# Performance work log

Measured on AMD Instinct MI355X. Metric: run time of the kernel, lower is better.

Reference implementation:

```python
import jax, jax.numpy as jnp
import numpy as np

B, N, QD = 1, 4096, 1024
H, DH = 16, 64  # heads, dim_head; inner_dim = H*DH = 1024
SCALE = DH ** -0.5


def setup_inputs() -> dict:
    key = jax.random.key(0)
    ks = jax.random.split(key, 6)
    inner = H * DH
    return {
        "x": jax.random.normal(ks[0], (B, N, QD), dtype=jnp.float32),
        "Wq": jax.random.normal(ks[1], (QD, inner), dtype=jnp.float32) * (QD ** -0.5),
        "Wk": jax.random.normal(ks[2], (QD, inner), dtype=jnp.float32) * (QD ** -0.5),
        "Wv": jax.random.normal(ks[3], (QD, inner), dtype=jnp.float32) * (QD ** -0.5),
        "Wo": jax.random.normal(ks[4], (inner, QD), dtype=jnp.float32) * (inner ** -0.5),
        "bo": jnp.zeros((QD,), dtype=jnp.float32),
    }


def reference(x, Wq, Wk, Wv, Wo, bo):
    b, n, _ = x.shape
    # projections, split heads: b n (h d) -> b h n d
    q = (x @ Wq).reshape(b, n, H, DH).transpose(0, 2, 1, 3)
    k = (x @ Wk).reshape(b, n, H, DH).transpose(0, 2, 1, 3)
    v = (x @ Wv).reshape(b, n, H, DH).transpose(0, 2, 1, 3)
    # fp32-forced QK^T (ATTN_PRECISION='fp32' path), then scale
    sim = jnp.einsum("bhid,bhjd->bhij", q.astype(jnp.float32), k.astype(jnp.float32)) * SCALE
    attn = jax.nn.softmax(sim, axis=-1)
    out = jnp.einsum("bhij,bhjd->bhid", attn, v)  # b h n d
    out = out.transpose(0, 2, 1, 3).reshape(b, n, H * DH)  # merge heads
    return out @ Wo + bo
```

## Files before the change

### kernel.cpp

```cpp
#include <hip/hip_runtime.h>
#include <stdint.h>

#define NH 16
#define NN 4096

typedef __attribute__((ext_vector_type(8))) short bf16x8;
typedef __attribute__((ext_vector_type(4))) short bf16x4;
typedef __attribute__((ext_vector_type(4))) float f32x4;
typedef __attribute__((ext_vector_type(16))) float f32x16;
typedef unsigned short u16;
typedef unsigned int u32;
typedef __attribute__((ext_vector_type(4))) u32 u32x4;

__device__ __forceinline__ u16 f2bf(float f) {
  u32 u = __float_as_uint(f);
  return (u16)((u + 0x7FFFu + ((u >> 16) & 1u)) >> 16);
}

#define GLD16(gp, lp)                                              \
  __builtin_amdgcn_global_load_lds(                                \
      (__attribute__((address_space(1))) void*)(gp),               \
      (__attribute__((address_space(3))) void*)(lp), 16, 0, 0)

__global__ __launch_bounds__(256) void prep(const float* __restrict__ x,
                                            const float* __restrict__ Wq,
                                            const float* __restrict__ Wk,
                                            const float* __restrict__ Wv,
                                            const float* __restrict__ Wo,
                                            u16* __restrict__ xb,
                                            u16* __restrict__ Wqt, u16* __restrict__ Wkt,
                                            u16* __restrict__ Wvt, u16* __restrict__ Wot) {
  __shared__ float tile[64][65];
  int z = blockIdx.z;
  int tid = threadIdx.x;
  if (z >= 4) {
    int bi = (z - 4) * 256 + blockIdx.y * 16 + blockIdx.x;
    size_t base = (size_t)bi * 8192;
#pragma unroll
    for (int k = 0; k < 4; ++k) {
      size_t i = base + (size_t)k * 2048 + tid * 8;
      float4 a = *(const float4*)(x + i);
      float4 b = *(const float4*)(x + i + 4);
      uint4 o;
      o.x = (u32)f2bf(a.x) | ((u32)f2bf(a.y) << 16);
      o.y = (u32)f2bf(a.z) | ((u32)f2bf(a.w) << 16);
      o.z = (u32)f2bf(b.x) | ((u32)f2bf(b.y) << 16);
      o.w = (u32)f2bf(b.z) | ((u32)f2bf(b.w) << 16);
      *(uint4*)(xb + i) = o;
    }
    return;
  }
  const float* src;
  u16* dst;
  float scale = 1.0f;
  if (z == 0) { src = Wq; dst = Wqt; scale = 0.125f * 1.4426950408889634f; }
  else if (z == 1) { src = Wk; dst = Wkt; }
  else if (z == 2) { src = Wv; dst = Wvt; }
  else { src = Wo; dst = Wot; }
  int tx = tid & 63, ty = tid >> 6;
  int c0 = blockIdx.x * 64, r0 = blockIdx.y * 64;
#pragma unroll
  for (int i = ty; i < 64; i += 4)
    tile[i][tx] = src[(size_t)(r0 + i) * 1024 + c0 + tx];
  __syncthreads();
#pragma unroll
  for (int i = ty; i < 64; i += 4)
    dst[(size_t)(c0 + i) * 1024 + r0 + tx] = f2bf(tile[tx][i] * scale);
}

__global__ __launch_bounds__(256) void gemm_qkv(const u16* __restrict__ A,
                                                const u16* __restrict__ Bt,
                                                u16* __restrict__ Qb, u16* __restrict__ Kb,
                                                u16* __restrict__ Vth) {
  __shared__ __align__(16) u16 SH[16384];
  u16* A_lds = SH;
  u16* B_lds = SH + 8192;
  const int tid = threadIdx.x;
  const int l = tid & 63, w = tid >> 6;
  const int g = l >> 4, c = l & 15;
  const int wr = w >> 1, wc = w & 1;
  const int m0 = blockIdx.y * 128, n0 = blockIdx.x * 128;

  const int srow = tid >> 2;
  const u32 sswz = (u32)(((tid & 3) * 16) ^ ((srow & 3) << 4));
  const char* Ag = (const char*)A + (size_t)(m0 + srow) * 2048 + sswz;
  const char* Bg = (const char*)Bt + (size_t)(n0 + srow) * 2048 + sswz;
  const u32 ldsb = (u32)(w * 1024);

#define GSTAGE(buf, ks_)                                                          \
  do {                                                                            \
    u32 koff_ = (u32)(ks_) * 64;                                                  \
    _Pragma("unroll") for (int p_ = 0; p_ < 2; ++p_) {                            \
      GLD16(Ag + koff_ + (size_t)p_ * 64 * 2048,                                  \
            (char*)A_lds + (buf) * 8192 + p_ * 4096 + ldsb);                      \
      GLD16(Bg + koff_ + (size_t)p_ * 64 * 2048,                                  \
            (char*)B_lds + (buf) * 8192 + p_ * 4096 + ldsb);                      \
    }                                                                             \
  } while (0)

  f32x4 acc[4][4];
#pragma unroll
  for (int i = 0; i < 4; ++i)
#pragma unroll
    for (int j = 0; j < 4; ++j) acc[i][j] = (f32x4){0.f, 0.f, 0.f, 0.f};

  int cur = 0;
  GSTAGE(0, 0);
  for (int ks = 0; ks < 32; ++ks) {
    GSTAGE(cur ^ 1, (ks + 1) & 31);
    asm volatile("s_waitcnt vmcnt(4)" ::: "memory");
    __builtin_amdgcn_s_barrier();
    __builtin_amdgcn_sched_barrier(0);
    const char* Ac = (const char*)A_lds + cur * 8192;
    const char* Bc = (const char*)B_lds + cur * 8192;
    bf16x8 af[4], bfr[4];
#pragma unroll
    for (int i = 0; i < 4; ++i) {
      int row = wr * 64 + i * 16 + c;
      af[i] = *(const bf16x8*)(Ac + row * 64 + ((g * 16) ^ ((row & 3) << 4)));
    }
#pragma unroll
    for (int j = 0; j < 4; ++j) {
      int row = wc * 64 + j * 16 + c;
      bfr[j] = *(const bf16x8*)(Bc + row * 64 + ((g * 16) ^ ((row & 3) << 4)));
    }
    __builtin_amdgcn_s_setprio(1);
#pragma unroll
    for (int i = 0; i < 4; ++i)
#pragma unroll
      for (int j = 0; j < 4; ++j)
        acc[i][j] = __builtin_amdgcn_mfma_f32_16x16x32_bf16(af[i], bfr[j], acc[i][j], 0, 0, 0);
    __builtin_amdgcn_s_setprio(0);
    asm volatile("s_waitcnt lgkmcnt(0)" ::: "memory");
    __builtin_amdgcn_s_barrier();
    __builtin_amdgcn_sched_barrier(0);
    cur ^= 1;
  }
#undef GSTAGE

  const int sec = n0 >> 10;
  if (sec < 2) {
#pragma unroll
    for (int i = 0; i < 4; ++i)
#pragma unroll
      for (int j = 0; j < 4; ++j)
#pragma unroll
        for (int r = 0; r < 4; ++r) {
          int m = m0 + wr * 64 + i * 16 + g * 4 + r;
          int cc = (n0 + wc * 64 + j * 16 + c) & 1023;
          u16 v = f2bf(acc[i][j][r]);
          if (sec == 0) Qb[(size_t)m * 1024 + cc] = v;
          else Kb[(size_t)m * 1024 + cc] = v;
        }
  } else {
    const int gq = ((g & 1) << 1) | (g >> 1);
    const int cc0 = n0 & 1023;
#pragma unroll
    for (int i = 0; i < 4; ++i)
#pragma unroll
      for (int j = 0; j < 4; ++j)
#pragma unroll
        for (int r = 0; r < 4; ++r) {
          int cl = wc * 64 + j * 16 + c;
          int mql = wr * 64 + i * 16 + gq * 4 + r;
          SH[cl * 128 + (mql ^ ((cl & 15) << 3))] = f2bf(acc[i][j][r]);
        }
    __syncthreads();
#pragma unroll
    for (int p = 0; p < 4; ++p) {
      int row = p * 32 + (tid >> 3);
#pragma unroll
      for (int half = 0; half < 2; ++half) {
        int mq = (tid & 7) * 8 + half * 64;
        bf16x8 vv = *(const bf16x8*)&SH[row * 128 + (mq ^ ((row & 15) << 3))];
        *(bf16x8*)(Vth + (size_t)(cc0 + row) * 4096 + m0 + mq) = vv;
      }
    }
  }
}

__global__ __launch_bounds__(256) void gemm_out128(const u16* __restrict__ A,
                                                   const u16* __restrict__ Bt,
                                                   float* __restrict__ out,
                                                   const float* __restrict__ bias) {
  __shared__ __align__(16) u16 A_lds[2][128 * 32];
  __shared__ __align__(16) u16 B_lds[2][64 * 32];
  const int tid = threadIdx.x;
  const int l = tid & 63, w = tid >> 6;
  const int g = l >> 4, c = l & 15;
  const int m0 = blockIdx.y * 128, n0 = blockIdx.x * 64;

  const int srow = tid >> 2;
  const u32 sswz = (u32)(((tid & 3) * 16) ^ ((srow & 3) << 4));
  const char* Ag = (const char*)A + (size_t)(m0 + srow) * 2048 + sswz;
  const char* Bg = (const char*)Bt + (size_t)(n0 + srow) * 2048 + sswz;
  const u32 ldsb = (u32)(w * 1024);

#define GSTAGE3(buf, ks_)                                                         \
  do {                                                                            \
    u32 koff_ = (u32)(ks_) * 64;                                                  \
    GLD16(Ag + koff_, (char*)A_lds[buf] + ldsb);                                  \
    GLD16(Ag + koff_ + (size_t)64 * 2048, (char*)A_lds[buf] + 4096 + ldsb);       \
    GLD16(Bg + koff_, (char*)B_lds[buf] + ldsb);                                  \
  } while (0)

  f32x4 acc[2][4];
#pragma unroll
  for (int i = 0; i < 2; ++i)
#pragma unroll
    for (int j = 0; j < 4; ++j) acc[i][j] = (f32x4){0.f, 0.f, 0.f, 0.f};

  int cur = 0;
  GSTAGE3(0, 0);
  for (int ks = 0; ks < 32; ++ks) {
    GSTAGE3(cur ^ 1, (ks + 1) & 31);
    asm volatile("s_waitcnt vmcnt(3)" ::: "memory");
    __builtin_amdgcn_s_barrier();
    __builtin_amdgcn_sched_barrier(0);
    const char* Ac = (const char*)A_lds[cur];
    const char* Bc = (const char*)B_lds[cur];
    bf16x8 af[2], bfr[4];
#pragma unroll
    for (int i = 0; i < 2; ++i) {
      int row = w * 32 + i * 16 + c;
      af[i] = *(const bf16x8*)(Ac + row * 64 + ((g * 16) ^ ((row & 3) << 4)));
    }
#pragma unroll
    for (int j = 0; j < 4; ++j) {
      int row = j * 16 + c;
      bfr[j] = *(const bf16x8*)(Bc + row * 64 + ((g * 16) ^ ((row & 3) << 4)));
    }
    __builtin_amdgcn_s_setprio(1);
#pragma unroll
    for (int i = 0; i < 2; ++i)
#pragma unroll
      for (int j = 0; j < 4; ++j)
        acc[i][j] = __builtin_amdgcn_mfma_f32_16x16x32_bf16(af[i], bfr[j], acc[i][j], 0, 0, 0);
    __builtin_amdgcn_s_setprio(0);
    asm volatile("s_waitcnt lgkmcnt(0)" ::: "memory");
    __builtin_amdgcn_s_barrier();
    __builtin_amdgcn_sched_barrier(0);
    cur ^= 1;
  }
#undef GSTAGE3

#pragma unroll
  for (int i = 0; i < 2; ++i)
#pragma unroll
    for (int j = 0; j < 4; ++j)
#pragma unroll
      for (int r = 0; r < 4; ++r) {
        int m = m0 + w * 32 + i * 16 + g * 4 + r;
        int col = n0 + j * 16 + c;
        out[(size_t)m * 1024 + col] = acc[i][j][r] + bias[col];
      }
}

template <int SPLIT>
__global__ __launch_bounds__(256, 2) void flash_attn_t(const u16* __restrict__ Qb,
                                                       const u16* __restrict__ Kb,
                                                       const u16* __restrict__ Vt,
                                                       u16* __restrict__ Ob,
                                                       float* __restrict__ Op,
                                                       float* __restrict__ Lp) {
  constexpr int NT = SPLIT ? 32 : 64;
  __shared__ __align__(16) u16 K_lds[2][64 * 64];
  __shared__ __align__(16) u16 V_lds[2][64 * 64];
  const int tid = threadIdx.x;
  const int l = tid & 63, w = tid >> 6;
  const int lq = l & 31, hi = l >> 5;
  const int h = blockIdx.y;
  const int z = SPLIT ? blockIdx.z : 0;
  const int kb = z * 32;
  const int qb = blockIdx.x * 256 + w * 64;
  const int q0 = qb + lq, q1 = qb + 32 + lq;

  bf16x8 qf0[4], qf1[4];
  {
    const u16* qr0 = Qb + (size_t)q0 * 1024 + h * 64;
    const u16* qr1 = Qb + (size_t)q1 * 1024 + h * 64;
#pragma unroll
    for (int dm = 0; dm < 4; ++dm) {
      qf0[dm] = *(const bf16x8*)(qr0 + dm * 16 + hi * 8);
      qf1[dm] = *(const bf16x8*)(qr1 + dm * 16 + hi * 8);
    }
  }

  f32x16 ot0[2], ot1[2];
#pragma unroll
  for (int a = 0; a < 2; ++a)
#pragma unroll
    for (int r = 0; r < 16; ++r) { ot0[a][r] = 0.f; ot1[a][r] = 0.f; }
  float lrow0 = 0.f, lrow1 = 0.f;
  u32 pkA0[16], pkA1[16], pkB0[16], pkB1[16];

  const int srow = tid >> 3;
  const u32 sswz = (u32)(((tid & 7) * 16) ^ ((srow & 7) << 4));
  const char* Kg = (const char*)Kb + ((size_t)srow * 1024 + h * 64) * 2 + sswz;
  const char* Vg = (const char*)Vt + ((size_t)(h * 64 + srow) * 4096) * 2 + sswz;
  const u32 ldsb = (u32)(w * 1024);

#define PVONLY(P0, P1, VSLOT)                                                     \
  {                                                                               \
    const char* Vp_ = (const char*)(VSLOT);                                       \
    __builtin_amdgcn_s_setprio(1);                                                \
    _Pragma("unroll") for (int sti_ = 0; sti_ < 4; ++sti_) {                      \
      u32x4 pw0_ = {P0[sti_ * 4 + 0], P0[sti_ * 4 + 1], P0[sti_ * 4 + 2],         \
                    P0[sti_ * 4 + 3]};                                            \
      u32x4 pw1_ = {P1[sti_ * 4 + 0], P1[sti_ * 4 + 1], P1[sti_ * 4 + 2],         \
                    P1[sti_ * 4 + 3]};                                            \
      bf16x8 pf0_ = __builtin_bit_cast(bf16x8, pw0_);                             \
      bf16x8 pf1_ = __builtin_bit_cast(bf16x8, pw1_);                             \
      const u32 cb_ = (u32)(sti_ * 32 + hi * 16);                                 \
      _Pragma("unroll") for (int a_ = 0; a_ < 2; ++a_) {                          \
        const int rowd_ = a_ * 32 + lq;                                           \
        const u32 rs_ = (u32)(rowd_ * 128), rz_ = (u32)((rowd_ & 7) << 4);        \
        bf16x8 vf_ = *(const bf16x8*)(Vp_ + rs_ + (cb_ ^ rz_));                   \
        ot0[a_] = __builtin_amdgcn_mfma_f32_32x32x16_bf16(vf_, pf0_, ot0[a_], 0, 0, 0); \
        ot1[a_] = __builtin_amdgcn_mfma_f32_32x32x16_bf16(vf_, pf1_, ot1[a_], 0, 0, 0); \
      }                                                                           \
    }                                                                             \
    __builtin_amdgcn_s_setprio(0);                                                \
  }

#define BODY(TI, C0, C1, P0, P1, DOPREV)                                          \
  {                                                                               \
    const int ti_ = (TI);                                                         \
    const int nxt_ = (ti_ + 1) & (NT - 1);                                        \
    {                                                                             \
      const char* kg_ = Kg + (size_t)(kb + nxt_) * 64 * 2048;                     \
      char* kl_ = (char*)K_lds[nxt_ & 1] + ldsb;                                  \
      GLD16(kg_, kl_);                                                            \
      GLD16(kg_ + 32 * 2048, kl_ + 4096);                                         \
      const char* vg_ = Vg + (size_t)(kb + ti_) * 128;                            \
      char* vl_ = (char*)V_lds[ti_ & 1] + ldsb;                                   \
      GLD16(vg_, vl_);                                                            \
      GLD16(vg_ + (size_t)32 * 8192, vl_ + 4096);                                 \
    }                                                                             \
    asm volatile("s_waitcnt vmcnt(4)" ::: "memory");                              \
    __builtin_amdgcn_s_barrier();                                                 \
    __builtin_amdgcn_sched_barrier(0);                                            \
    const char* Kc_ = (const char*)K_lds[ti_ & 1];                                \
    f32x16 st0_[2], st1_[2];                                                      \
    _Pragma("unroll") for (int s_ = 0; s_ < 2; ++s_)                              \
    _Pragma("unroll") for (int r_ = 0; r_ < 16; ++r_) {                           \
      st0_[s_][r_] = 0.f;                                                         \
      st1_[s_][r_] = 0.f;                                                         \
    }                                                                             \
    __builtin_amdgcn_s_setprio(1);                                                \
    _Pragma("unroll") for (int s_ = 0; s_ < 2; ++s_) {                            \
      const int row_ = s_ * 32 + lq;                                              \
      const u32 rs_ = (u32)(row_ * 128), rz_ = (u32)((row_ & 7) << 4);            \
      _Pragma("unroll") for (int dm_ = 0; dm_ < 4; ++dm_) {                       \
        bf16x8 kf_ = *(const bf16x8*)(Kc_ + rs_ + ((u32)(dm_ * 32 + hi * 16) ^ rz_)); \
        st0_[s_] = __builtin_amdgcn_mfma_f32_32x32x16_bf16(kf_, qf0[dm_], st0_[s_], 0, 0, 0); \
        st1_[s_] = __builtin_amdgcn_mfma_f32_32x32x16_bf16(kf_, qf1[dm_], st1_[s_], 0, 0, 0); \
      }                                                                           \
    }                                                                             \
    __builtin_amdgcn_s_setprio(0);                                                \
    if (DOPREV) PVONLY(P0, P1, V_lds[(ti_ - 1) & 1]);                             \
    float rs0_ = 0.f, rs1_ = 0.f;                                                 \
    _Pragma("unroll") for (int s_ = 0; s_ < 2; ++s_)                              \
    _Pragma("unroll") for (int j_ = 0; j_ < 8; ++j_) {                            \
      float a0_ = __builtin_amdgcn_exp2f(st0_[s_][2 * j_]);                       \
      float a1_ = __builtin_amdgcn_exp2f(st0_[s_][2 * j_ + 1]);                   \
      rs0_ += a0_ + a1_;                                                          \
      u32 wp0_;                                                                   \
      asm("v_cvt_pk_bf16_f32 %0, %1, %2" : "=v"(wp0_) : "v"(a0_), "v"(a1_));      \
      C0[s_ * 8 + j_] = wp0_;                                                     \
      float b0_ = __builtin_amdgcn_exp2f(st1_[s_][2 * j_]);                       \
      float b1_ = __builtin_amdgcn_exp2f(st1_[s_][2 * j_ + 1]);                   \
      rs1_ += b0_ + b1_;                                                          \
      u32 wp1_;                                                                   \
      asm("v_cvt_pk_bf16_f32 %0, %1, %2" : "=v"(wp1_) : "v"(b0_), "v"(b1_));      \
      C1[s_ * 8 + j_] = wp1_;                                                     \
    }                                                                             \
    lrow0 += rs0_;                                                                \
    lrow1 += rs1_;                                                                \
    asm volatile("s_waitcnt lgkmcnt(0)" ::: "memory");                            \
    __builtin_amdgcn_s_barrier();                                                 \
    __builtin_amdgcn_sched_barrier(0);                                            \
  }

  {
    const char* kg0 = Kg + (size_t)kb * 64 * 2048;
    char* kl = (char*)K_lds[0] + ldsb;
    GLD16(kg0, kl);
    GLD16(kg0 + 32 * 2048, kl + 4096);
  }

  BODY(0, pkA0, pkA1, pkA0, pkA1, 0);
  for (int i = 1; i < NT - 1; i += 2) {
    BODY(i, pkB0, pkB1, pkA0, pkA1, 1);
    BODY(i + 1, pkA0, pkA1, pkB0, pkB1, 1);
  }
  BODY(NT - 1, pkB0, pkB1, pkA0, pkA1, 1);
  asm volatile("s_waitcnt vmcnt(0)" ::: "memory");
  __builtin_amdgcn_s_barrier();
  __builtin_amdgcn_sched_barrier(0);
  PVONLY(pkB0, pkB1, V_lds[(NT - 1) & 1]);

#undef BODY
#undef PVONLY

  lrow0 += __shfl_xor(lrow0, 32, 64);
  lrow1 += __shfl_xor(lrow1, 32, 64);
  if constexpr (SPLIT) {
    float* or0 = Op + (size_t)z * (4096 * 1024) + (size_t)q0 * 1024 + h * 64 + hi * 4;
    float* or1 = Op + (size_t)z * (4096 * 1024) + (size_t)q1 * 1024 + h * 64 + hi * 4;
#pragma unroll
    for (int a = 0; a < 2; ++a)
#pragma unroll
      for (int rr = 0; rr < 4; ++rr) {
        float4 f0 = {ot0[a][rr * 4 + 0], ot0[a][rr * 4 + 1], ot0[a][rr * 4 + 2],
                     ot0[a][rr * 4 + 3]};
        *(float4*)(or0 + a * 32 + rr * 8) = f0;
        float4 f1 = {ot1[a][rr * 4 + 0], ot1[a][rr * 4 + 1], ot1[a][rr * 4 + 2],
                     ot1[a][rr * 4 + 3]};
        *(float4*)(or1 + a * 32 + rr * 8) = f1;
      }
    if (hi == 0) {
      Lp[z * 65536 + h * 4096 + q0] = lrow0;
      Lp[z * 65536 + h * 4096 + q1] = lrow1;
    }
  } else {
    float inv0 = 1.f / lrow0, inv1 = 1.f / lrow1;
    u16* or0 = Ob + (size_t)q0 * 1024 + h * 64 + hi * 4;
    u16* or1 = Ob + (size_t)q1 * 1024 + h * 64 + hi * 4;
#pragma unroll
    for (int a = 0; a < 2; ++a)
#pragma unroll
      for (int rr = 0; rr < 4; ++rr) {
        ushort4 o4;
        o4.x = f2bf(ot0[a][rr * 4 + 0] * inv0);
        o4.y = f2bf(ot0[a][rr * 4 + 1] * inv0);
        o4.z = f2bf(ot0[a][rr * 4 + 2] * inv0);
        o4.w = f2bf(ot0[a][rr * 4 + 3] * inv0);
        *(ushort4*)(or0 + a * 32 + rr * 8) = o4;
        o4.x = f2bf(ot1[a][rr * 4 + 0] * inv1);
        o4.y = f2bf(ot1[a][rr * 4 + 1] * inv1);
        o4.z = f2bf(ot1[a][rr * 4 + 2] * inv1);
        o4.w = f2bf(ot1[a][rr * 4 + 3] * inv1);
        *(ushort4*)(or1 + a * 32 + rr * 8) = o4;
      }
  }
}

__global__ __launch_bounds__(256) void merge_halves(const float* __restrict__ O0,
                                                    const float* __restrict__ O1,
                                                    const float* __restrict__ L0,
                                                    const float* __restrict__ L1,
                                                    u16* __restrict__ Ob) {
  int idx = blockIdx.x * 256 + threadIdx.x;
  int q = idx >> 7;
  int c0 = (idx & 127) * 8;
  int h = c0 >> 6;
  float inv = 1.f / (L0[h * 4096 + q] + L1[h * 4096 + q]);
  size_t off = (size_t)q * 1024 + c0;
  float4 a0 = *(const float4*)(O0 + off), a1 = *(const float4*)(O0 + off + 4);
  float4 b0 = *(const float4*)(O1 + off), b1 = *(const float4*)(O1 + off + 4);
  ushort4 o0, o1;
  o0.x = f2bf((a0.x + b0.x) * inv);
  o0.y = f2bf((a0.y + b0.y) * inv);
  o0.z = f2bf((a0.z + b0.z) * inv);
  o0.w = f2bf((a0.w + b0.w) * inv);
  o1.x = f2bf((a1.x + b1.x) * inv);
  o1.y = f2bf((a1.y + b1.y) * inv);
  o1.z = f2bf((a1.z + b1.z) * inv);
  o1.w = f2bf((a1.w + b1.w) * inv);
  *(ushort4*)(Ob + off) = o0;
  *(ushort4*)(Ob + off + 4) = o1;
}

extern "C" void kernel_launch(void* const* d_in, const int* in_sizes, int n_in,
                              void* d_out, int out_size, void* d_ws, size_t ws_size,
                              hipStream_t stream) {
  const float* x = (const float*)d_in[0];
  const float* Wq = (const float*)d_in[1];
  const float* Wk = (const float*)d_in[2];
  const float* Wv = (const float*)d_in[3];
  const float* Wo = (const float*)d_in[4];
  const float* bo = (const float*)d_in[5];
  float* out = (float*)d_out;

  char* ws = (char*)d_ws;
  u16* xb  = (u16*)(ws);
  u16* Wqt = (u16*)(ws + (8u << 20));
  u16* Wot = (u16*)(ws + (14u << 20));
  u16* Qb  = (u16*)(ws + (16u << 20));
  u16* Kbf = (u16*)(ws + (24u << 20));
  u16* Vth = (u16*)(ws + (32u << 20));
  u16* Ob  = (u16*)(ws + (40u << 20));
  float* Op = (float*)(ws + (40u << 20));
  float* Lp = (float*)(ws + (72u << 20));
  u16* Wkt = Wqt + (1u << 20);
  u16* Wvt = Wqt + (2u << 20);

  const bool split = ws_size >= ((73u << 20) + (1u << 19));

  prep<<<dim3(16, 16, 6), 256, 0, stream>>>(x, Wq, Wk, Wv, Wo, xb, Wqt, Wkt, Wvt, Wot);
  gemm_qkv<<<dim3(24, 32), 256, 0, stream>>>(xb, Wqt, Qb, Kbf, Vth);

  if (split) {
    flash_attn_t<1><<<dim3(16, 16, 2), 256, 0, stream>>>(Qb, Kbf, Vth, nullptr, Op, Lp);
    u16* ObM = (u16*)ws;
    merge_halves<<<2048, 256, 0, stream>>>(Op, Op + (1u << 22), Lp, Lp + 65536, ObM);
    gemm_out128<<<dim3(16, 32), 256, 0, stream>>>(ObM, Wot, out, bo);
  } else {
    flash_attn_t<0><<<dim3(16, 16, 1), 256, 0, stream>>>(Qb, Kbf, Vth, Ob, nullptr, nullptr);
    gemm_out128<<<dim3(16, 32), 256, 0, stream>>>(Ob, Wot, out, bo);
  }
}
```

Measured before the change: 162.4 us.

## Fuse split-K attention merge into output GEMM and remap attention block order

Drops the separate merge_halves kernel. The output projection GEMM now reads the two fp32 partial attention outputs and their row sums directly, then combines, normalises and converts them to bf16 while staging its A tile into LDS. This saves one launch and the write and reread of the bf16 intermediate. The cost is that every N-tile block of the GEMM reloads the fp32 partials, which is 16x redundant global traffic, and does more ALU work inside the GEMM loop. Separately, the flash attention grid uses a new block-index swizzle that interleaves heads and splits across groups of 8, likely to spread K/V reuse across XCDs.

```diff
diff --git a/kernel.cpp b/kernel.cpp
--- a/kernel.cpp
+++ b/kernel.cpp
@@ -256,6 +256,135 @@
       }
 }
 
+__global__ __launch_bounds__(256) void gemm_out128f(const float* __restrict__ O0,
+                                                    const float* __restrict__ O1,
+                                                    const float* __restrict__ L0,
+                                                    const float* __restrict__ L1,
+                                                    const u16* __restrict__ Bt,
+                                                    float* __restrict__ out,
+                                                    const float* __restrict__ bias) {
+  __shared__ __align__(16) u16 A_lds[2][128 * 32];
+  __shared__ __align__(16) u16 B_lds[2][64 * 32];
+  const int tid = threadIdx.x;
+  const int l = tid & 63, w = tid >> 6;
+  const int g = l >> 4, c = l & 15;
+  const int m0 = blockIdx.y * 128, n0 = blockIdx.x * 64;
+
+  const int srow = tid >> 2;
+  const int chunk = tid & 3;
+  const int cidx = chunk ^ (srow & 3);
+  const u32 sswz = (u32)(((tid & 3) * 16) ^ ((srow & 3) << 4));
+  const char* Bg = (const char*)Bt + (size_t)(n0 + srow) * 2048 + sswz;
+  const u32 ldsb = (u32)(w * 1024);
+
+  float4 va0, va1, vb0, vb1, wa0, wa1, wb0, wb1;
+  float l0a, l1a, l0b, l1b;
+
+#define A_LOAD(KSN)                                                               \
+  {                                                                               \
+    int k0n_ = (KSN) * 32, hn_ = (KSN) >> 1;                                      \
+    const float* p0a_ = O0 + (size_t)(m0 + srow) * 1024 + k0n_ + cidx * 8;        \
+    const float* p0b_ = O0 + (size_t)(m0 + srow + 64) * 1024 + k0n_ + cidx * 8;   \
+    const float* p1a_ = O1 + (size_t)(m0 + srow) * 1024 + k0n_ + cidx * 8;        \
+    const float* p1b_ = O1 + (size_t)(m0 + srow + 64) * 1024 + k0n_ + cidx * 8;   \
+    va0 = *(const float4*)(p0a_);                                                 \
+    va1 = *(const float4*)(p0a_ + 4);                                             \
+    vb0 = *(const float4*)(p0b_);                                                 \
+    vb1 = *(const float4*)(p0b_ + 4);                                             \
+    wa0 = *(const float4*)(p1a_);                                                 \
+    wa1 = *(const float4*)(p1a_ + 4);                                             \
+    wb0 = *(const float4*)(p1b_);                                                 \
+    wb1 = *(const float4*)(p1b_ + 4);                                             \
+    l0a = L0[hn_ * 4096 + m0 + srow];                                             \
+    l1a = L1[hn_ * 4096 + m0 + srow];                                             \
+    l0b = L0[hn_ * 4096 + m0 + srow + 64];                                        \
+    l1b = L1[hn_ * 4096 + m0 + srow + 64];                                        \
+  }
+
+#define A_WRITE(BUF)                                                              \
+  {                                                                               \
+    float inva_ = 1.f / (l0a + l1a);                                              \
+    float invb_ = 1.f / (l0b + l1b);                                              \
+    uint4 pa_, pb_;                                                               \
+    pa_.x = (u32)f2bf((va0.x + wa0.x) * inva_) |                                  \
+            ((u32)f2bf((va0.y + wa0.y) * inva_) << 16);                           \
+    pa_.y = (u32)f2bf((va0.z + wa0.z) * inva_) |                                  \
+            ((u32)f2bf((va0.w + wa0.w) * inva_) << 16);                           \
+    pa_.z = (u32)f2bf((va1.x + wa1.x) * inva_) |                                  \
+            ((u32)f2bf((va1.y + wa1.y) * inva_) << 16);                           \
+    pa_.w = (u32)f2bf((va1.z + wa1.z) * inva_) |                                  \
+            ((u32)f2bf((va1.w + wa1.w) * inva_) << 16);                           \
+    pb_.x = (u32)f2bf((vb0.x + wb0.x) * invb_) |                                  \
+            ((u32)f2bf((vb0.y + wb0.y) * invb_) << 16);                           \
+    pb_.y = (u32)f2bf((vb0.z + wb0.z) * invb_) |                                  \
+            ((u32)f2bf((vb0.w + wb0.w) * invb_) << 16);                           \
+    pb_.z = (u32)f2bf((vb1.x + wb1.x) * invb_) |                                  \
+            ((u32)f2bf((vb1.y + wb1.y) * invb_) << 16);                           \
+    pb_.w = (u32)f2bf((vb1.z + wb1.z) * invb_) |                                  \
+            ((u32)f2bf((vb1.w + wb1.w) * invb_) << 16);                           \
+    *(uint4*)((char*)A_lds[BUF] + srow * 64 + chunk * 16) = pa_;                  \
+    *(uint4*)((char*)A_lds[BUF] + 4096 + srow * 64 + chunk * 16) = pb_;           \
+  }
+
+  f32x4 acc[2][4];
+#pragma unroll
+  for (int i = 0; i < 2; ++i)
+#pragma unroll
+    for (int j = 0; j < 4; ++j) acc[i][j] = (f32x4){0.f, 0.f, 0.f, 0.f};
+
+  GLD16(Bg, (char*)B_lds[0] + ldsb);
+  A_LOAD(0);
+  A_WRITE(0);
+
+  int cur = 0;
+  for (int ks = 0; ks < 32; ++ks) {
+    int ksn = (ks + 1) & 31;
+    GLD16(Bg + (u32)ksn * 64, (char*)B_lds[cur ^ 1] + ldsb);
+    A_LOAD(ksn);
+    asm volatile("s_waitcnt vmcnt(13) lgkmcnt(0)" ::: "memory");
+    __builtin_amdgcn_s_barrier();
+    __builtin_amdgcn_sched_barrier(0);
+    const char* Ac = (const char*)A_lds[cur];
+    const char* Bc = (const char*)B_lds[cur];
+    bf16x8 af[2], bfr[4];
+#pragma unroll
+    for (int i = 0; i < 2; ++i) {
+      int row = w * 32 + i * 16 + c;
+      af[i] = *(const bf16x8*)(Ac + row * 64 + ((g * 16) ^ ((row & 3) << 4)));
+    }
+#pragma unroll
+    for (int j = 0; j < 4; ++j) {
+      int row = j * 16 + c;
+      bfr[j] = *(const bf16x8*)(Bc + row * 64 + ((g * 16) ^ ((row & 3) << 4)));
+    }
+    __builtin_amdgcn_s_setprio(1);
+#pragma unroll
+    for (int i = 0; i < 2; ++i)
+#pragma unroll
+      for (int j = 0; j < 4; ++j)
+        acc[i][j] = __builtin_amdgcn_mfma_f32_16x16x32_bf16(af[i], bfr[j], acc[i][j], 0, 0, 0);
+    __builtin_amdgcn_s_setprio(0);
+    A_WRITE(cur ^ 1);
+    asm volatile("s_waitcnt lgkmcnt(0)" ::: "memory");
+    __builtin_amdgcn_s_barrier();
+    __builtin_amdgcn_sched_barrier(0);
+    cur ^= 1;
+  }
+#undef A_LOAD
+#undef A_WRITE
+
+#pragma unroll
+  for (int i = 0; i < 2; ++i)
+#pragma unroll
+    for (int j = 0; j < 4; ++j)
+#pragma unroll
+      for (int r = 0; r < 4; ++r) {
+        int m = m0 + w * 32 + i * 16 + g * 4 + r;
+        int col = n0 + j * 16 + c;
+        out[(size_t)m * 1024 + col] = acc[i][j][r] + bias[col];
+      }
+}
+
 template <int SPLIT>
 __global__ __launch_bounds__(256, 2) void flash_attn_t(const u16* __restrict__ Qb,
                                                        const u16* __restrict__ Kb,
@@ -269,10 +398,13 @@
   const int tid = threadIdx.x;
   const int l = tid & 63, w = tid >> 6;
   const int lq = l & 31, hi = l >> 5;
-  const int h = blockIdx.y;
-  const int z = SPLIT ? blockIdx.z : 0;
+  constexpr int CPX = SPLIT ? 64 : 32;
+  const int flat = blockIdx.x + (blockIdx.y << 4) + (blockIdx.z << 8);
+  const int p = (flat & 7) * CPX + (flat >> 3);
+  const int h = (p >> 4) & 15;
+  const int z = SPLIT ? (p >> 8) : 0;
   const int kb = z * 32;
-  const int qb = blockIdx.x * 256 + w * 64;
+  const int qb = (p & 15) * 256 + w * 64;
   const int q0 = qb + lq, q1 = qb + 32 + lq;
 
   bf16x8 qf0[4], qf1[4];
@@ -446,32 +578,6 @@
   }
 }
 
-__global__ __launch_bounds__(256) void merge_halves(const float* __restrict__ O0,
-                                                    const float* __restrict__ O1,
-                                                    const float* __restrict__ L0,
-                                                    const float* __restrict__ L1,
-                                                    u16* __restrict__ Ob) {
-  int idx = blockIdx.x * 256 + threadIdx.x;
-  int q = idx >> 7;
-  int c0 = (idx & 127) * 8;
-  int h = c0 >> 6;
-  float inv = 1.f / (L0[h * 4096 + q] + L1[h * 4096 + q]);
-  size_t off = (size_t)q * 1024 + c0;
-  float4 a0 = *(const float4*)(O0 + off), a1 = *(const float4*)(O0 + off + 4);
-  float4 b0 = *(const float4*)(O1 + off), b1 = *(const float4*)(O1 + off + 4);
-  ushort4 o0, o1;
-  o0.x = f2bf((a0.x + b0.x) * inv);
-  o0.y = f2bf((a0.y + b0.y) * inv);
-  o0.z = f2bf((a0.z + b0.z) * inv);
-  o0.w = f2bf((a0.w + b0.w) * inv);
-  o1.x = f2bf((a1.x + b1.x) * inv);
-  o1.y = f2bf((a1.y + b1.y) * inv);
-  o1.z = f2bf((a1.z + b1.z) * inv);
-  o1.w = f2bf((a1.w + b1.w) * inv);
-  *(ushort4*)(Ob + off) = o0;
-  *(ushort4*)(Ob + off + 4) = o1;
-}
-
 extern "C" void kernel_launch(void* const* d_in, const int* in_sizes, int n_in,
                               void* d_out, int out_size, void* d_ws, size_t ws_size,
                               hipStream_t stream) {
@@ -503,9 +609,8 @@
 
   if (split) {
     flash_attn_t<1><<<dim3(16, 16, 2), 256, 0, stream>>>(Qb, Kbf, Vth, nullptr, Op, Lp);
-    u16* ObM = (u16*)ws;
-    merge_halves<<<2048, 256, 0, stream>>>(Op, Op + (1u << 22), Lp, Lp + 65536, ObM);
-    gemm_out128<<<dim3(16, 32), 256, 0, stream>>>(ObM, Wot, out, bo);
+    gemm_out128f<<<dim3(16, 32), 256, 0, stream>>>(Op, Op + (1u << 22), Lp, Lp + 65536,
+                                                   Wot, out, bo);
   } else {
     flash_attn_t<0><<<dim3(16, 16, 1), 256, 0, stream>>>(Qb, Kbf, Vth, Ob, nullptr, nullptr);
     gemm_out128<<<dim3(16, 32), 256, 0, stream>>>(Ob, Wot, out, bo);
```

New measurement: 182.4 us. 1.12x slower.
